# Performance work log

Hardware: AMD Instinct MI355X
Metric: run time of the kernel (lower is better)

## Reference

```python
import jax, jax.numpy as jnp
import numpy as np

B, S, D_IN, D_H, DEPTH = 4, 2048, 1024, 1024, 1024


def setup_inputs() -> dict:
    key = jax.random.key(0)
    ks = jax.random.split(key, 11)
    s = 1.0 / np.sqrt(D_IN)
    sh = 1.0 / np.sqrt(D_H)
    return {
        "query": jax.random.normal(ks[0], (B, S, D_IN), jnp.float32),
        "keys": jax.random.normal(ks[1], (B, S, D_IN), jnp.float32),
        "values": jax.random.normal(ks[2], (B, S, D_IN), jnp.float32),
        "Wq": jax.random.normal(ks[3], (D_IN, D_H), jnp.float32) * s,
        "bq": jax.random.normal(ks[4], (D_H,), jnp.float32) * s,
        "Wk": jax.random.normal(ks[5], (D_IN, D_H), jnp.float32) * s,
        "bk": jax.random.normal(ks[6], (D_H,), jnp.float32) * s,
        "Wv": jax.random.normal(ks[7], (D_IN, D_H), jnp.float32) * s,
        "bv": jax.random.normal(ks[8], (D_H,), jnp.float32) * s,
        "Wd": jax.random.normal(ks[9], (D_H, DEPTH), jnp.float32) * sh,
        "bd": jax.random.normal(ks[10], (DEPTH,), jnp.float32) * sh,
    }


def reference(query, keys, values, Wq, bq, Wk, bk, Wv, bv, Wd, bd):
    q = jnp.einsum("bsd,dh->bsh", query, Wq) + bq
    k = jnp.einsum("bsd,dh->bsh", keys, Wk) + bk
    v = jnp.einsum("bsd,dh->bsh", values, Wv) + bv
    # NOTE: source has no 1/sqrt(d) scaling
    scores = jnp.einsum("bqh,bkh->bqk", q, k)  # [B, S, S]
    attn = jax.nn.softmax(scores, axis=-1)
    attended = jnp.einsum("bqk,bkh->bqh", attn, v)
    return jnp.einsum("bsh,hd->bsd", attended, Wd) + bd
```

## Files before the change

kernel.cpp:

```cpp
#include <hip/hip_runtime.h>
#include <stdint.h>

#define BM 128
#define BN 128
#define BK 64
#define TILE_ELEMS (128 * 64)

typedef _Float16 f16;
typedef __attribute__((ext_vector_type(8))) _Float16 f16x8;
typedef __attribute__((ext_vector_type(4))) _Float16 f16x4;
typedef __attribute__((ext_vector_type(4))) float floatx4;

static __device__ __forceinline__ void async_load16(const void* g, void* l) {
    __builtin_amdgcn_global_load_lds(
        (const __attribute__((address_space(1))) unsigned int*)g,
        (__attribute__((address_space(3))) unsigned int*)l, 16, 0, 0);
}

static __device__ __forceinline__ void stage_tile(const f16* src, int ld, f16* lds, int tid) {
    int lane = tid & 63;
    int wbase = (tid >> 6) * 64;
#pragma unroll
    for (int t = 0; t < 4; ++t) {
        int c = wbase + t * 256 + lane;
        int r = c >> 3, ck = c & 7;
        const f16* gp = src + (size_t)r * ld + ((ck ^ (r & 7)) << 3);
        f16* lp = lds + (size_t)(wbase + t * 256) * 8;
        async_load16(gp, lp);
    }
}

static __device__ __forceinline__ f16x8 frag(const f16* lds, int row, int kblk) {
    return *(const f16x8*)(lds + (((row << 3) + (kblk ^ (row & 7))) << 3));
}

template <int CMODE>
static __device__ __forceinline__ void gemm_body(
    f16* As, f16* Bs,
    const f16* Ap, int lda, long long a_zoff,
    const f16* Bp, int ldb, long long b_zoff,
    void* Cp, int ldc, long long c_zoff,
    const float* bias, int K, int z)
{
    int tid = threadIdx.x;
    int lane = tid & 63;
    int wid = tid >> 6;
    int wm = wid >> 1, wn = wid & 1;

    int gx = gridDim.x;
    int nwg = gx * gridDim.y;
    int bid = blockIdx.y * gx + blockIdx.x;
    if ((nwg & 7) == 0) {
        int chunk = nwg >> 3;
        bid = (bid & 7) * chunk + (bid >> 3);
    }
    int bx = bid % gx;
    int by = bid / gx;

    size_t row0 = (size_t)by * BM;
    size_t col0 = (size_t)bx * BN;

    floatx4 acc[4][4];
#pragma unroll
    for (int i = 0; i < 4; ++i)
#pragma unroll
        for (int j = 0; j < 4; ++j) acc[i][j] = floatx4{0.f, 0.f, 0.f, 0.f};

    const f16* a0 = Ap + (size_t)z * a_zoff + row0 * lda;
    const f16* b0 = Bp + (size_t)z * b_zoff + col0 * ldb;

    int quad = lane >> 4, mr = lane & 15;

    for (int k0 = 0; k0 < K; k0 += BK) {
        __syncthreads();
        stage_tile(a0 + k0, lda, As, tid);
        stage_tile(b0 + k0, ldb, Bs, tid);
        __syncthreads();

#pragma unroll
        for (int s = 0; s < 2; ++s) {
            f16x8 ah[4];
#pragma unroll
            for (int i = 0; i < 4; ++i) ah[i] = frag(As, wm * 64 + i * 16 + mr, s * 4 + quad);
#pragma unroll
            for (int j = 0; j < 4; ++j) {
                f16x8 bh = frag(Bs, wn * 64 + j * 16 + mr, s * 4 + quad);
#pragma unroll
                for (int i = 0; i < 4; ++i)
                    acc[i][j] = __builtin_amdgcn_mfma_f32_16x16x32_f16(ah[i], bh, acc[i][j], 0, 0, 0);
            }
        }
    }

#pragma unroll
    for (int i = 0; i < 4; ++i) {
#pragma unroll
        for (int j = 0; j < 4; ++j) {
#pragma unroll
            for (int r = 0; r < 4; ++r) {
                size_t rr = row0 + (size_t)(wm * 64 + i * 16 + quad * 4 + r);
                size_t cc = col0 + (size_t)(wn * 64 + j * 16 + mr);
                float v = acc[i][j][r];
                if (bias) v += bias[cc];
                if constexpr (CMODE == 0) {
                    float* C = (float*)Cp + (size_t)z * c_zoff;
                    C[rr * ldc + cc] = v;
                } else if constexpr (CMODE == 1) {
                    f16* C = (f16*)Cp + (size_t)z * c_zoff;
                    C[rr * ldc + cc] = (f16)v;
                } else {
                    f16* C = (f16*)Cp;
                    size_t b = rr >> 11, s = rr & 2047;
                    C[((b << 10) + cc) * 2048 + s] = (f16)v;
                }
            }
        }
    }
}

#define DECL_SMEM                                        \
    __shared__ __align__(16) f16 smem[2 * TILE_ELEMS];   \
    f16* As = smem;                                      \
    f16* Bs = smem + TILE_ELEMS;

__global__ __launch_bounds__(256, 2) void g_qkv(const f16* x, const f16* W,
                                                f16* qk, f16* vT,
                                                const float* bq, const float* bk,
                                                const float* bv, int D, long long ten) {
    DECL_SMEM
    int z = blockIdx.z;
    const float* bias = (z == 0) ? bq : (z == 1) ? bk : bv;
    if (z < 2) {
        gemm_body<1>(As, Bs, x + (size_t)z * ten, D, 0, W + (size_t)z * D * D, D, 0,
                     qk + (size_t)z * ten, D, 0, bias, D, 0);
    } else {
        gemm_body<3>(As, Bs, x + (size_t)2 * ten, D, 0, W + (size_t)2 * D * D, D, 0,
                     vT, 0, 0, bias, D, 0);
    }
}
__global__ __launch_bounds__(256, 2) void g_scores(const f16* A, int lda, long long az,
                                                   const f16* B, int ldb, long long bz,
                                                   float* C, int ldc, long long cz, int K) {
    DECL_SMEM
    gemm_body<0>(As, Bs, A, lda, az, B, ldb, bz, C, ldc, cz, nullptr, K, blockIdx.z);
}
__global__ __launch_bounds__(256, 2) void g_attnv(const f16* A, int lda, long long az,
                                                  const f16* B, int ldb, long long bz,
                                                  f16* C, int ldc, long long cz, int K) {
    DECL_SMEM
    gemm_body<1>(As, Bs, A, lda, az, B, ldb, bz, C, ldc, cz, nullptr, K, blockIdx.z);
}
__global__ __launch_bounds__(256, 2) void g_out(const f16* A, int lda, const f16* B, int ldb,
                                                float* C, int ldc, const float* bias, int K) {
    DECL_SMEM
    gemm_body<0>(As, Bs, A, lda, 0, B, ldb, 0, C, ldc, 0, bias, K, 0);
}

__global__ __launch_bounds__(256) void cvt_f16(const float* q, const float* k, const float* v,
                                               f16* dst, long long ten) {
    int z = blockIdx.y;
    const float* src = (z == 0) ? q : (z == 1) ? k : v;
    size_t i = ((size_t)blockIdx.x * 256 + threadIdx.x) * 4;
    float4 x = *(const float4*)(src + i);
    f16x4 h = {(f16)x.x, (f16)x.y, (f16)x.z, (f16)x.w};
    *(f16x4*)(dst + (size_t)z * ten + i) = h;
}

__global__ __launch_bounds__(256) void wtrans(const float* Wq, const float* Wk,
                                              const float* Wv, const float* Wd,
                                              f16* T, int n) {
    __shared__ float tile[32][33];
    int z = blockIdx.z;
    const float* W = (z == 0) ? Wq : (z == 1) ? Wk : (z == 2) ? Wv : Wd;
    f16* Tz = T + (size_t)z * n * n;
    int bx = blockIdx.x * 32;
    int by = blockIdx.y * 32;
    int tx = threadIdx.x & 31;
    int ty = threadIdx.x >> 5;
    for (int r = ty; r < 32; r += 8) tile[r][tx] = W[(size_t)(by + r) * n + bx + tx];
    __syncthreads();
    for (int r = ty; r < 32; r += 8) Tz[(size_t)(bx + r) * n + by + tx] = (f16)tile[tx][r];
}

__global__ __launch_bounds__(256) void softmax_k(float* scores) {
    size_t row = blockIdx.x;
    float* rp = scores + row * 2048;
    int tid = threadIdx.x;
    int lane = tid & 63, w = tid >> 6;
    float x[8];
    float mx = -3.4e38f;
#pragma unroll
    for (int i = 0; i < 8; ++i) {
        x[i] = rp[tid + i * 256];
        mx = fmaxf(mx, x[i]);
    }
#pragma unroll
    for (int o = 32; o > 0; o >>= 1) mx = fmaxf(mx, __shfl_xor(mx, o, 64));
    __shared__ float redm[4];
    __shared__ float reds[4];
    if (lane == 0) redm[w] = mx;
    __syncthreads();
    mx = fmaxf(fmaxf(redm[0], redm[1]), fmaxf(redm[2], redm[3]));
    float s = 0.f;
#pragma unroll
    for (int i = 0; i < 8; ++i) {
        x[i] = __expf(x[i] - mx);
        s += x[i];
    }
#pragma unroll
    for (int o = 32; o > 0; o >>= 1) s += __shfl_xor(s, o, 64);
    if (lane == 0) reds[w] = s;
    __syncthreads();
    s = reds[0] + reds[1] + reds[2] + reds[3];
    float inv = 1.f / s;
    f16* op = (f16*)rp;
#pragma unroll
    for (int i = 0; i < 8; ++i) op[tid + i * 256] = (f16)(x[i] * inv);
}

extern "C" void kernel_launch(void* const* d_in, const int* in_sizes, int n_in,
                              void* d_out, int out_size, void* d_ws, size_t ws_size,
                              hipStream_t stream) {
    const float* query  = (const float*)d_in[0];
    const float* keys   = (const float*)d_in[1];
    const float* values = (const float*)d_in[2];
    const float* Wq = (const float*)d_in[3];
    const float* bq = (const float*)d_in[4];
    const float* Wk = (const float*)d_in[5];
    const float* bk = (const float*)d_in[6];
    const float* Wv = (const float*)d_in[7];
    const float* bv = (const float*)d_in[8];
    const float* Wd = (const float*)d_in[9];
    const float* bd = (const float*)d_in[10];
    float* out = (float*)d_out;

    const int S = 2048, D = 1024, NB = 4;
    const size_t TEN = (size_t)NB * S * D;

    char* p = (char*)d_ws;
    auto alloc = [&](size_t bytes) {
        char* r = p;
        p += (bytes + 255) & ~(size_t)255;
        return r;
    };
    f16* x3  = (f16*)alloc(TEN * 2 * 3);
    f16* q16 = (f16*)alloc(TEN * 2 * 2);
    f16* k16 = q16 + TEN;
    f16* vT  = (f16*)alloc(TEN * 2);
    f16* WT  = (f16*)alloc((size_t)D * D * 2 * 4);
    float* scores = (float*)p;
    long long avail = (long long)ws_size - (long long)(p - (char*)d_ws);
    long long sbytes = (long long)S * S * 4;
    int g = (avail >= 4 * sbytes) ? 4 : (avail >= 2 * sbytes) ? 2 : 1;
    f16* att = x3;

    dim3 blk(256);
    cvt_f16<<<dim3((unsigned)(TEN / 1024), 3), blk, 0, stream>>>(query, keys, values, x3, TEN);
    wtrans<<<dim3(D / 32, D / 32, 4), blk, 0, stream>>>(Wq, Wk, Wv, Wd, WT, D);

    g_qkv<<<dim3(D / BN, (NB * S) / BM, 3), blk, 0, stream>>>(
        x3, WT, q16, vT, bq, bk, bv, D, (long long)TEN);

    for (int g0 = 0; g0 < NB; g0 += g) {
        int gz = (NB - g0 < g) ? (NB - g0) : g;
        dim3 sgrid(S / BN, S / BM, gz);
        g_scores<<<sgrid, blk, 0, stream>>>(
            q16 + (size_t)g0 * S * D, D, (long long)S * D,
            k16 + (size_t)g0 * S * D, D, (long long)S * D,
            scores, S, (long long)S * S, D);
        softmax_k<<<dim3((unsigned)(gz * S)), blk, 0, stream>>>(scores);
        dim3 agrid(D / BN, S / BM, gz);
        g_attnv<<<agrid, blk, 0, stream>>>(
            (const f16*)scores, 2 * S, (long long)S * 2 * S,
            vT + (size_t)g0 * D * S, S, (long long)D * S,
            att + (size_t)g0 * S * D, D, (long long)S * D, S);
    }

    g_out<<<dim3(D / BN, (NB * S) / BM, 1), blk, 0, stream>>>(att, D, WT + (size_t)3 * D * D, D,
                                                              out, D, bd, D);
}
```

Baseline: 359.4 us.

## Use 256x256 GEMM tiles with 8 waves and double-buffered LDS prefetch

Every GEMM kernel now uses 256x256 output tiles computed by 512 threads (8 waves, 2x4 layout), each wave holding a 128x64 accumulator block. The K loop double-buffers A and B tiles in LDS. It spreads the async global-to-LDS loads for the next tile across four compute phases and raises wave priority around the MFMA bursts. The goal is to hide global load latency and raise arithmetic intensity per LDS byte. In exchange it uses 128KB of LDS per block, and there are fewer workgroups: the output projection has only 128 blocks, which may leave CUs idle.

Measured after the change: 446.0 us. +24.1%, slower.

```diff
diff --git a/kernel.cpp b/kernel.cpp
--- a/kernel.cpp
+++ b/kernel.cpp
@@ -1,36 +1,34 @@
 #include <hip/hip_runtime.h>
 #include <stdint.h>
 
-#define BM 128
-#define BN 128
+#define BM 256
+#define BN 256
 #define BK 64
-#define TILE_ELEMS (128 * 64)
+#define TSTRIDE 32768
 
 typedef _Float16 f16;
 typedef __attribute__((ext_vector_type(8))) _Float16 f16x8;
 typedef __attribute__((ext_vector_type(4))) _Float16 f16x4;
 typedef __attribute__((ext_vector_type(4))) float floatx4;
 
+#define SBAR() asm volatile("s_barrier" ::: "memory")
+#define WAITV0() asm volatile("s_waitcnt vmcnt(0)" ::: "memory")
+
 static __device__ __forceinline__ void async_load16(const void* g, void* l) {
     __builtin_amdgcn_global_load_lds(
         (const __attribute__((address_space(1))) unsigned int*)g,
         (__attribute__((address_space(3))) unsigned int*)l, 16, 0, 0);
 }
 
-static __device__ __forceinline__ void stage_tile(const f16* src, int ld, f16* lds, int tid) {
-    int lane = tid & 63;
-    int wbase = (tid >> 6) * 64;
-#pragma unroll
-    for (int t = 0; t < 4; ++t) {
-        int c = wbase + t * 256 + lane;
-        int r = c >> 3, ck = c & 7;
-        const f16* gp = src + (size_t)r * ld + ((ck ^ (r & 7)) << 3);
-        f16* lp = lds + (size_t)(wbase + t * 256) * 8;
-        async_load16(gp, lp);
-    }
-}
-
-static __device__ __forceinline__ f16x8 frag(const f16* lds, int row, int kblk) {
+static __device__ __forceinline__ void stage256(const f16* src, int ld, f16* lds, int tid, int chunk) {
+    int c = (chunk << 9) + tid;
+    int r = c >> 3, ck = c & 7;
+    const f16* gp = src + (size_t)r * ld + ((ck ^ (r & 7)) << 3);
+    f16* lp = lds + (size_t)((chunk << 9) + (tid & ~63)) * 8;
+    async_load16(gp, lp);
+}
+
+static __device__ __forceinline__ f16x8 frag256(const f16* lds, int row, int kblk) {
     return *(const f16x8*)(lds + (((row << 3) + (kblk ^ (row & 7))) << 3));
 }
 
@@ -45,7 +43,7 @@
     int tid = threadIdx.x;
     int lane = tid & 63;
     int wid = tid >> 6;
-    int wm = wid >> 1, wn = wid & 1;
+    int wm = wid >> 2, wn = wid & 3;
 
     int gx = gridDim.x;
     int nwg = gx * gridDim.y;
@@ -56,13 +54,12 @@
     }
     int bx = bid % gx;
     int by = bid / gx;
-
     size_t row0 = (size_t)by * BM;
     size_t col0 = (size_t)bx * BN;
 
-    floatx4 acc[4][4];
-#pragma unroll
-    for (int i = 0; i < 4; ++i)
+    floatx4 acc[8][4];
+#pragma unroll
+    for (int i = 0; i < 8; ++i)
 #pragma unroll
         for (int j = 0; j < 4; ++j) acc[i][j] = floatx4{0.f, 0.f, 0.f, 0.f};
 
@@ -70,35 +67,75 @@
     const f16* b0 = Bp + (size_t)z * b_zoff + col0 * ldb;
 
     int quad = lane >> 4, mr = lane & 15;
-
-    for (int k0 = 0; k0 < K; k0 += BK) {
-        __syncthreads();
-        stage_tile(a0 + k0, lda, As, tid);
-        stage_tile(b0 + k0, ldb, Bs, tid);
-        __syncthreads();
-
-#pragma unroll
-        for (int s = 0; s < 2; ++s) {
-            f16x8 ah[4];
-#pragma unroll
-            for (int i = 0; i < 4; ++i) ah[i] = frag(As, wm * 64 + i * 16 + mr, s * 4 + quad);
-#pragma unroll
-            for (int j = 0; j < 4; ++j) {
-                f16x8 bh = frag(Bs, wn * 64 + j * 16 + mr, s * 4 + quad);
+    int NT = K >> 6;
+
+#pragma unroll
+    for (int c = 0; c < 4; ++c) stage256(a0, lda, As, tid, c);
+#pragma unroll
+    for (int c = 0; c < 4; ++c) stage256(b0, ldb, Bs, tid, c);
+    WAITV0();
+    SBAR();
+
+    for (int kt = 0; kt < NT; ++kt) {
+        int cur = kt & 1;
+        f16* Acur = As + cur * TSTRIDE;
+        f16* Bcur = Bs + cur * TSTRIDE;
+        f16* Anxt = As + (cur ^ 1) * TSTRIDE;
+        f16* Bnxt = Bs + (cur ^ 1) * TSTRIDE;
+        const f16* an = a0 + (size_t)(kt + 1) * BK;
+        const f16* bn = b0 + (size_t)(kt + 1) * BK;
+        bool pf = (kt + 1 < NT);
+
+#pragma unroll
+        for (int p = 0; p < 4; ++p) {
+            const int mh = p >> 1, nh = p & 1;
+            f16x8 af[2][4], bf[2][2];
+#pragma unroll
+            for (int s = 0; s < 2; ++s) {
 #pragma unroll
                 for (int i = 0; i < 4; ++i)
-                    acc[i][j] = __builtin_amdgcn_mfma_f32_16x16x32_f16(ah[i], bh, acc[i][j], 0, 0, 0);
+                    af[s][i] = frag256(Acur, wm * 128 + mh * 64 + i * 16 + mr, s * 4 + quad);
+#pragma unroll
+                for (int j = 0; j < 2; ++j)
+                    bf[s][j] = frag256(Bcur, wn * 64 + nh * 32 + j * 16 + mr, s * 4 + quad);
             }
+            if (pf) {
+                if (p == 0) {
+                    stage256(an, lda, Anxt, tid, 0);
+                    stage256(an, lda, Anxt, tid, 1);
+                    stage256(an, lda, Anxt, tid, 2);
+                } else if (p == 1) {
+                    stage256(an, lda, Anxt, tid, 3);
+                    stage256(bn, ldb, Bnxt, tid, 0);
+                    stage256(bn, ldb, Bnxt, tid, 1);
+                } else if (p == 2) {
+                    stage256(bn, ldb, Bnxt, tid, 2);
+                    stage256(bn, ldb, Bnxt, tid, 3);
+                }
+            }
+            SBAR();
+            __builtin_amdgcn_s_setprio(1);
+#pragma unroll
+            for (int s = 0; s < 2; ++s)
+#pragma unroll
+                for (int j = 0; j < 2; ++j)
+#pragma unroll
+                    for (int i = 0; i < 4; ++i)
+                        acc[mh * 4 + i][nh * 2 + j] = __builtin_amdgcn_mfma_f32_16x16x32_f16(
+                            af[s][i], bf[s][j], acc[mh * 4 + i][nh * 2 + j], 0, 0, 0);
+            __builtin_amdgcn_s_setprio(0);
+            if (p == 3 && pf) WAITV0();
+            SBAR();
         }
     }
 
 #pragma unroll
-    for (int i = 0; i < 4; ++i) {
+    for (int i = 0; i < 8; ++i) {
 #pragma unroll
         for (int j = 0; j < 4; ++j) {
 #pragma unroll
             for (int r = 0; r < 4; ++r) {
-                size_t rr = row0 + (size_t)(wm * 64 + i * 16 + quad * 4 + r);
+                size_t rr = row0 + (size_t)(wm * 128 + i * 16 + quad * 4 + r);
                 size_t cc = col0 + (size_t)(wn * 64 + j * 16 + mr);
                 float v = acc[i][j][r];
                 if (bias) v += bias[cc];
@@ -118,12 +155,12 @@
     }
 }
 
-#define DECL_SMEM                                        \
-    __shared__ __align__(16) f16 smem[2 * TILE_ELEMS];   \
-    f16* As = smem;                                      \
-    f16* Bs = smem + TILE_ELEMS;
-
-__global__ __launch_bounds__(256, 2) void g_qkv(const f16* x, const f16* W,
+#define DECL_SMEM                                      \
+    __shared__ __align__(16) f16 smem[2 * TSTRIDE];    \
+    f16* As = smem;                                    \
+    f16* Bs = smem + 16384;
+
+__global__ __launch_bounds__(512, 2) void g_qkv(const f16* x, const f16* W,
                                                 f16* qk, f16* vT,
                                                 const float* bq, const float* bk,
                                                 const float* bv, int D, long long ten) {
@@ -138,19 +175,19 @@
                      vT, 0, 0, bias, D, 0);
     }
 }
-__global__ __launch_bounds__(256, 2) void g_scores(const f16* A, int lda, long long az,
+__global__ __launch_bounds__(512, 2) void g_scores(const f16* A, int lda, long long az,
                                                    const f16* B, int ldb, long long bz,
                                                    float* C, int ldc, long long cz, int K) {
     DECL_SMEM
     gemm_body<0>(As, Bs, A, lda, az, B, ldb, bz, C, ldc, cz, nullptr, K, blockIdx.z);
 }
-__global__ __launch_bounds__(256, 2) void g_attnv(const f16* A, int lda, long long az,
+__global__ __launch_bounds__(512, 2) void g_attnv(const f16* A, int lda, long long az,
                                                   const f16* B, int ldb, long long bz,
                                                   f16* C, int ldc, long long cz, int K) {
     DECL_SMEM
     gemm_body<1>(As, Bs, A, lda, az, B, ldb, bz, C, ldc, cz, nullptr, K, blockIdx.z);
 }
-__global__ __launch_bounds__(256, 2) void g_out(const f16* A, int lda, const f16* B, int ldb,
+__global__ __launch_bounds__(512, 2) void g_out(const f16* A, int lda, const f16* B, int ldb,
                                                 float* C, int ldc, const float* bias, int K) {
     DECL_SMEM
     gemm_body<0>(As, Bs, A, lda, 0, B, ldb, 0, C, ldc, 0, bias, K, 0);
@@ -255,27 +292,28 @@
     f16* att = x3;
 
     dim3 blk(256);
+    dim3 blk512(512);
     cvt_f16<<<dim3((unsigned)(TEN / 1024), 3), blk, 0, stream>>>(query, keys, values, x3, TEN);
     wtrans<<<dim3(D / 32, D / 32, 4), blk, 0, stream>>>(Wq, Wk, Wv, Wd, WT, D);
 
-    g_qkv<<<dim3(D / BN, (NB * S) / BM, 3), blk, 0, stream>>>(
+    g_qkv<<<dim3(D / BN, (NB * S) / BM, 3), blk512, 0, stream>>>(
         x3, WT, q16, vT, bq, bk, bv, D, (long long)TEN);
 
     for (int g0 = 0; g0 < NB; g0 += g) {
         int gz = (NB - g0 < g) ? (NB - g0) : g;
         dim3 sgrid(S / BN, S / BM, gz);
-        g_scores<<<sgrid, blk, 0, stream>>>(
+        g_scores<<<sgrid, blk512, 0, stream>>>(
             q16 + (size_t)g0 * S * D, D, (long long)S * D,
             k16 + (size_t)g0 * S * D, D, (long long)S * D,
             scores, S, (long long)S * S, D);
         softmax_k<<<dim3((unsigned)(gz * S)), blk, 0, stream>>>(scores);
         dim3 agrid(D / BN, S / BM, gz);
-        g_attnv<<<agrid, blk, 0, stream>>>(
+        g_attnv<<<agrid, blk512, 0, stream>>>(
             (const f16*)scores, 2 * S, (long long)S * 2 * S,
             vT + (size_t)g0 * D * S, S, (long long)D * S,
             att + (size_t)g0 * S * D, D, (long long)S * D, S);
     }
 
-    g_out<<<dim3(D / BN, (NB * S) / BM, 1), blk, 0, stream>>>(att, D, WT + (size_t)3 * D * D, D,
-                                                              out, D, bd, D);
-}
+    g_out<<<dim3(D / BN, (NB * S) / BM, 1), blk512, 0, stream>>>(att, D, WT + (size_t)3 * D * D, D,
+                                                                 out, D, bd, D);
+}
```

## Triple-buffer GEMM K-loop with async LDS loads and 256x128 tiles

Applied to the files above, without the earlier changes.

Replaces the two-barrier, single-buffer K loop with a three-stage ring of LDS buffers. Global-to-LDS loads for tile k+2 are issued while tile k is being computed, and explicit vmcnt waits plus a single s_barrier per iteration gate each stage. The block tile grows to 256x128 with 512 threads (8 waves), and fragments are preloaded before an MFMA burst that runs at raised wave priority. This aims to hide global load latency and halve barrier count, at the cost of about 147KB of LDS per block, which limits occupancy to one block per CU and halves the grid size.

Result: slower. 383.7 us (+6.8%).

```diff
diff --git a/kernel.cpp b/kernel.cpp
--- a/kernel.cpp
+++ b/kernel.cpp
@@ -1,33 +1,34 @@
 #include <hip/hip_runtime.h>
 #include <stdint.h>
 
-#define BM 128
+#define BM 256
 #define BN 128
 #define BK 64
-#define TILE_ELEMS (128 * 64)
+#define ATILE (BM * BK)
+#define BTILE (BN * BK)
+#define BUFSTRIDE (ATILE + BTILE)
 
 typedef _Float16 f16;
 typedef __attribute__((ext_vector_type(8))) _Float16 f16x8;
 typedef __attribute__((ext_vector_type(4))) _Float16 f16x4;
 typedef __attribute__((ext_vector_type(4))) float floatx4;
 
+#define SBAR() asm volatile("s_barrier" ::: "memory")
+#define WAITV6() asm volatile("s_waitcnt vmcnt(6)" ::: "memory")
+#define WAITV0() asm volatile("s_waitcnt vmcnt(0)" ::: "memory")
+
 static __device__ __forceinline__ void async_load16(const void* g, void* l) {
     __builtin_amdgcn_global_load_lds(
         (const __attribute__((address_space(1))) unsigned int*)g,
         (__attribute__((address_space(3))) unsigned int*)l, 16, 0, 0);
 }
 
-static __device__ __forceinline__ void stage_tile(const f16* src, int ld, f16* lds, int tid) {
-    int lane = tid & 63;
-    int wbase = (tid >> 6) * 64;
-#pragma unroll
-    for (int t = 0; t < 4; ++t) {
-        int c = wbase + t * 256 + lane;
-        int r = c >> 3, ck = c & 7;
-        const f16* gp = src + (size_t)r * ld + ((ck ^ (r & 7)) << 3);
-        f16* lp = lds + (size_t)(wbase + t * 256) * 8;
-        async_load16(gp, lp);
-    }
+static __device__ __forceinline__ void stage_unit(const f16* src, int ld, f16* lds, int tid, int u) {
+    int c = (u << 9) + tid;
+    int r = c >> 3, ck = c & 7;
+    const f16* gp = src + (size_t)r * ld + ((ck ^ (r & 7)) << 3);
+    f16* lp = lds + (size_t)((u << 9) + (tid & ~63)) * 8;
+    async_load16(gp, lp);
 }
 
 static __device__ __forceinline__ f16x8 frag(const f16* lds, int row, int kblk) {
@@ -36,7 +37,7 @@
 
 template <int CMODE>
 static __device__ __forceinline__ void gemm_body(
-    f16* As, f16* Bs,
+    f16* smem,
     const f16* Ap, int lda, long long a_zoff,
     const f16* Bp, int ldb, long long b_zoff,
     void* Cp, int ldc, long long c_zoff,
@@ -56,7 +57,6 @@
     }
     int bx = bid % gx;
     int by = bid / gx;
-
     size_t row0 = (size_t)by * BM;
     size_t col0 = (size_t)bx * BN;
 
@@ -70,25 +70,54 @@
     const f16* b0 = Bp + (size_t)z * b_zoff + col0 * ldb;
 
     int quad = lane >> 4, mr = lane & 15;
-
-    for (int k0 = 0; k0 < K; k0 += BK) {
-        __syncthreads();
-        stage_tile(a0 + k0, lda, As, tid);
-        stage_tile(b0 + k0, ldb, Bs, tid);
-        __syncthreads();
-
+    int NT = K >> 6;
+
+    auto issue_tile = [&](int kt) {
+        f16* Ab = smem + (kt % 3) * BUFSTRIDE;
+        f16* Bb = Ab + ATILE;
+        const f16* an = a0 + (size_t)kt * BK;
+        const f16* bn = b0 + (size_t)kt * BK;
+        stage_unit(an, lda, Ab, tid, 0);
+        stage_unit(an, lda, Ab, tid, 1);
+        stage_unit(an, lda, Ab, tid, 2);
+        stage_unit(an, lda, Ab, tid, 3);
+        stage_unit(bn, ldb, Bb, tid, 0);
+        stage_unit(bn, ldb, Bb, tid, 1);
+    };
+
+    issue_tile(0);
+    issue_tile(1);
+    WAITV6();
+    SBAR();
+
+    for (int kt = 0; kt < NT; ++kt) {
+        f16* Ac = smem + (kt % 3) * BUFSTRIDE;
+        f16* Bc = Ac + ATILE;
+        if (kt + 2 < NT) issue_tile(kt + 2);
+
+        f16x8 af[2][4], bf[2][4];
 #pragma unroll
         for (int s = 0; s < 2; ++s) {
-            f16x8 ah[4];
-#pragma unroll
-            for (int i = 0; i < 4; ++i) ah[i] = frag(As, wm * 64 + i * 16 + mr, s * 4 + quad);
-#pragma unroll
-            for (int j = 0; j < 4; ++j) {
-                f16x8 bh = frag(Bs, wn * 64 + j * 16 + mr, s * 4 + quad);
+#pragma unroll
+            for (int i = 0; i < 4; ++i)
+                af[s][i] = frag(Ac, wm * 64 + i * 16 + mr, s * 4 + quad);
+#pragma unroll
+            for (int j = 0; j < 4; ++j)
+                bf[s][j] = frag(Bc, wn * 64 + j * 16 + mr, s * 4 + quad);
+        }
+        __builtin_amdgcn_s_setprio(1);
+#pragma unroll
+        for (int s = 0; s < 2; ++s)
+#pragma unroll
+            for (int j = 0; j < 4; ++j)
 #pragma unroll
                 for (int i = 0; i < 4; ++i)
-                    acc[i][j] = __builtin_amdgcn_mfma_f32_16x16x32_f16(ah[i], bh, acc[i][j], 0, 0, 0);
-            }
+                    acc[i][j] = __builtin_amdgcn_mfma_f32_16x16x32_f16(af[s][i], bf[s][j], acc[i][j], 0, 0, 0);
+        __builtin_amdgcn_s_setprio(0);
+
+        if (kt + 1 < NT) {
+            if (kt + 2 < NT) WAITV6(); else WAITV0();
+            SBAR();
         }
     }
 
@@ -118,12 +147,9 @@
     }
 }
 
-#define DECL_SMEM                                        \
-    __shared__ __align__(16) f16 smem[2 * TILE_ELEMS];   \
-    f16* As = smem;                                      \
-    f16* Bs = smem + TILE_ELEMS;
-
-__global__ __launch_bounds__(256, 2) void g_qkv(const f16* x, const f16* W,
+#define DECL_SMEM __shared__ __align__(16) f16 smem[3 * BUFSTRIDE];
+
+__global__ __launch_bounds__(512, 2) void g_qkv(const f16* x, const f16* W,
                                                 f16* qk, f16* vT,
                                                 const float* bq, const float* bk,
                                                 const float* bv, int D, long long ten) {
@@ -131,29 +157,29 @@
     int z = blockIdx.z;
     const float* bias = (z == 0) ? bq : (z == 1) ? bk : bv;
     if (z < 2) {
-        gemm_body<1>(As, Bs, x + (size_t)z * ten, D, 0, W + (size_t)z * D * D, D, 0,
+        gemm_body<1>(smem, x + (size_t)z * ten, D, 0, W + (size_t)z * D * D, D, 0,
                      qk + (size_t)z * ten, D, 0, bias, D, 0);
     } else {
-        gemm_body<3>(As, Bs, x + (size_t)2 * ten, D, 0, W + (size_t)2 * D * D, D, 0,
+        gemm_body<3>(smem, x + (size_t)2 * ten, D, 0, W + (size_t)2 * D * D, D, 0,
                      vT, 0, 0, bias, D, 0);
     }
 }
-__global__ __launch_bounds__(256, 2) void g_scores(const f16* A, int lda, long long az,
+__global__ __launch_bounds__(512, 2) void g_scores(const f16* A, int lda, long long az,
                                                    const f16* B, int ldb, long long bz,
                                                    float* C, int ldc, long long cz, int K) {
     DECL_SMEM
-    gemm_body<0>(As, Bs, A, lda, az, B, ldb, bz, C, ldc, cz, nullptr, K, blockIdx.z);
-}
-__global__ __launch_bounds__(256, 2) void g_attnv(const f16* A, int lda, long long az,
+    gemm_body<0>(smem, A, lda, az, B, ldb, bz, C, ldc, cz, nullptr, K, blockIdx.z);
+}
+__global__ __launch_bounds__(512, 2) void g_attnv(const f16* A, int lda, long long az,
                                                   const f16* B, int ldb, long long bz,
                                                   f16* C, int ldc, long long cz, int K) {
     DECL_SMEM
-    gemm_body<1>(As, Bs, A, lda, az, B, ldb, bz, C, ldc, cz, nullptr, K, blockIdx.z);
-}
-__global__ __launch_bounds__(256, 2) void g_out(const f16* A, int lda, const f16* B, int ldb,
+    gemm_body<1>(smem, A, lda, az, B, ldb, bz, C, ldc, cz, nullptr, K, blockIdx.z);
+}
+__global__ __launch_bounds__(512, 2) void g_out(const f16* A, int lda, const f16* B, int ldb,
                                                 float* C, int ldc, const float* bias, int K) {
     DECL_SMEM
-    gemm_body<0>(As, Bs, A, lda, 0, B, ldb, 0, C, ldc, 0, bias, K, 0);
+    gemm_body<0>(smem, A, lda, 0, B, ldb, 0, C, ldc, 0, bias, K, 0);
 }
 
 __global__ __launch_bounds__(256) void cvt_f16(const float* q, const float* k, const float* v,
@@ -255,27 +281,28 @@
     f16* att = x3;
 
     dim3 blk(256);
+    dim3 blk512(512);
     cvt_f16<<<dim3((unsigned)(TEN / 1024), 3), blk, 0, stream>>>(query, keys, values, x3, TEN);
     wtrans<<<dim3(D / 32, D / 32, 4), blk, 0, stream>>>(Wq, Wk, Wv, Wd, WT, D);
 
-    g_qkv<<<dim3(D / BN, (NB * S) / BM, 3), blk, 0, stream>>>(
+    g_qkv<<<dim3(D / BN, (NB * S) / BM, 3), blk512, 0, stream>>>(
         x3, WT, q16, vT, bq, bk, bv, D, (long long)TEN);
 
     for (int g0 = 0; g0 < NB; g0 += g) {
         int gz = (NB - g0 < g) ? (NB - g0) : g;
         dim3 sgrid(S / BN, S / BM, gz);
-        g_scores<<<sgrid, blk, 0, stream>>>(
+        g_scores<<<sgrid, blk512, 0, stream>>>(
             q16 + (size_t)g0 * S * D, D, (long long)S * D,
             k16 + (size_t)g0 * S * D, D, (long long)S * D,
             scores, S, (long long)S * S, D);
         softmax_k<<<dim3((unsigned)(gz * S)), blk, 0, stream>>>(scores);
         dim3 agrid(D / BN, S / BM, gz);
-        g_attnv<<<agrid, blk, 0, stream>>>(
+        g_attnv<<<agrid, blk512, 0, stream>>>(
             (const f16*)scores, 2 * S, (long long)S * 2 * S,
             vT + (size_t)g0 * D * S, S, (long long)D * S,
             att + (size_t)g0 * S * D, D, (long long)S * D, S);
     }
 
-    g_out<<<dim3(D / BN, (NB * S) / BM, 1), blk, 0, stream>>>(att, D, WT + (size_t)3 * D * D, D,
-                                                              out, D, bd, D);
-}
+    g_out<<<dim3(D / BN, (NB * S) / BM, 1), blk512, 0, stream>>>(att, D, WT + (size_t)3 * D * D, D,
+                                                                 out, D, bd, D);
+}
```

## Double-buffer GEMM LDS tiles and vectorize softmax row loads/stores

Applied to the files above, without the earlier changes.

The shared GEMM body now uses two LDS buffers, issuing async global-to-LDS loads for the next K tile while MFMAs run on the current one, with one barrier per iteration instead of two. LDS use per block doubles to 64 KB, which may limit the two-blocks-per-CU occupancy target. The softmax kernel also switches to contiguous per-thread float4 loads and f16x4 stores instead of strided scalar accesses. The in-place f16 write over the fp32 row is safe because of the barriers between the read and the write.

Result: slower. 374.3 us (+4.2%).

```diff
diff --git a/kernel.cpp b/kernel.cpp
--- a/kernel.cpp
+++ b/kernel.cpp
@@ -36,7 +36,7 @@
 
 template <int CMODE>
 static __device__ __forceinline__ void gemm_body(
-    f16* As, f16* Bs,
+    f16* smem,
     const f16* Ap, int lda, long long a_zoff,
     const f16* Bp, int ldb, long long b_zoff,
     void* Cp, int ldc, long long c_zoff,
@@ -71,25 +71,34 @@
 
     int quad = lane >> 4, mr = lane & 15;
 
-    for (int k0 = 0; k0 < K; k0 += BK) {
-        __syncthreads();
-        stage_tile(a0 + k0, lda, As, tid);
-        stage_tile(b0 + k0, ldb, Bs, tid);
-        __syncthreads();
+    stage_tile(a0, lda, smem, tid);
+    stage_tile(b0, ldb, smem + TILE_ELEMS, tid);
+    __syncthreads();
+
+    int kt = 0;
+    for (int k0 = 0; k0 < K; k0 += BK, ++kt) {
+        f16* Ac = smem + (kt & 1) * (2 * TILE_ELEMS);
+        f16* Bc = Ac + TILE_ELEMS;
+        if (k0 + BK < K) {
+            f16* An = smem + ((kt & 1) ^ 1) * (2 * TILE_ELEMS);
+            stage_tile(a0 + k0 + BK, lda, An, tid);
+            stage_tile(b0 + k0 + BK, ldb, An + TILE_ELEMS, tid);
+        }
 
 #pragma unroll
         for (int s = 0; s < 2; ++s) {
             f16x8 ah[4];
 #pragma unroll
-            for (int i = 0; i < 4; ++i) ah[i] = frag(As, wm * 64 + i * 16 + mr, s * 4 + quad);
+            for (int i = 0; i < 4; ++i) ah[i] = frag(Ac, wm * 64 + i * 16 + mr, s * 4 + quad);
 #pragma unroll
             for (int j = 0; j < 4; ++j) {
-                f16x8 bh = frag(Bs, wn * 64 + j * 16 + mr, s * 4 + quad);
+                f16x8 bh = frag(Bc, wn * 64 + j * 16 + mr, s * 4 + quad);
 #pragma unroll
                 for (int i = 0; i < 4; ++i)
                     acc[i][j] = __builtin_amdgcn_mfma_f32_16x16x32_f16(ah[i], bh, acc[i][j], 0, 0, 0);
             }
         }
+        __syncthreads();
     }
 
 #pragma unroll
@@ -118,10 +127,7 @@
     }
 }
 
-#define DECL_SMEM                                        \
-    __shared__ __align__(16) f16 smem[2 * TILE_ELEMS];   \
-    f16* As = smem;                                      \
-    f16* Bs = smem + TILE_ELEMS;
+#define DECL_SMEM __shared__ __align__(16) f16 smem[4 * TILE_ELEMS];
 
 __global__ __launch_bounds__(256, 2) void g_qkv(const f16* x, const f16* W,
                                                 f16* qk, f16* vT,
@@ -131,10 +137,10 @@
     int z = blockIdx.z;
     const float* bias = (z == 0) ? bq : (z == 1) ? bk : bv;
     if (z < 2) {
-        gemm_body<1>(As, Bs, x + (size_t)z * ten, D, 0, W + (size_t)z * D * D, D, 0,
+        gemm_body<1>(smem, x + (size_t)z * ten, D, 0, W + (size_t)z * D * D, D, 0,
                      qk + (size_t)z * ten, D, 0, bias, D, 0);
     } else {
-        gemm_body<3>(As, Bs, x + (size_t)2 * ten, D, 0, W + (size_t)2 * D * D, D, 0,
+        gemm_body<3>(smem, x + (size_t)2 * ten, D, 0, W + (size_t)2 * D * D, D, 0,
                      vT, 0, 0, bias, D, 0);
     }
 }
@@ -142,18 +148,18 @@
                                                    const f16* B, int ldb, long long bz,
                                                    float* C, int ldc, long long cz, int K) {
     DECL_SMEM
-    gemm_body<0>(As, Bs, A, lda, az, B, ldb, bz, C, ldc, cz, nullptr, K, blockIdx.z);
+    gemm_body<0>(smem, A, lda, az, B, ldb, bz, C, ldc, cz, nullptr, K, blockIdx.z);
 }
 __global__ __launch_bounds__(256, 2) void g_attnv(const f16* A, int lda, long long az,
                                                   const f16* B, int ldb, long long bz,
                                                   f16* C, int ldc, long long cz, int K) {
     DECL_SMEM
-    gemm_body<1>(As, Bs, A, lda, az, B, ldb, bz, C, ldc, cz, nullptr, K, blockIdx.z);
+    gemm_body<1>(smem, A, lda, az, B, ldb, bz, C, ldc, cz, nullptr, K, blockIdx.z);
 }
 __global__ __launch_bounds__(256, 2) void g_out(const f16* A, int lda, const f16* B, int ldb,
                                                 float* C, int ldc, const float* bias, int K) {
     DECL_SMEM
-    gemm_body<0>(As, Bs, A, lda, 0, B, ldb, 0, C, ldc, 0, bias, K, 0);
+    gemm_body<0>(smem, A, lda, 0, B, ldb, 0, C, ldc, 0, bias, K, 0);
 }
 
 __global__ __launch_bounds__(256) void cvt_f16(const float* q, const float* k, const float* v,
@@ -187,13 +193,12 @@
     float* rp = scores + row * 2048;
     int tid = threadIdx.x;
     int lane = tid & 63, w = tid >> 6;
-    float x[8];
+    const float4* rp4 = (const float4*)(rp + (size_t)tid * 8);
+    float4 a = rp4[0], b = rp4[1];
+    float x[8] = {a.x, a.y, a.z, a.w, b.x, b.y, b.z, b.w};
     float mx = -3.4e38f;
 #pragma unroll
-    for (int i = 0; i < 8; ++i) {
-        x[i] = rp[tid + i * 256];
-        mx = fmaxf(mx, x[i]);
-    }
+    for (int i = 0; i < 8; ++i) mx = fmaxf(mx, x[i]);
 #pragma unroll
     for (int o = 32; o > 0; o >>= 1) mx = fmaxf(mx, __shfl_xor(mx, o, 64));
     __shared__ float redm[4];
@@ -213,9 +218,11 @@
     __syncthreads();
     s = reds[0] + reds[1] + reds[2] + reds[3];
     float inv = 1.f / s;
-    f16* op = (f16*)rp;
-#pragma unroll
-    for (int i = 0; i < 8; ++i) op[tid + i * 256] = (f16)(x[i] * inv);
+    f16* op = (f16*)rp + (size_t)tid * 8;
+    f16x4 h0 = {(f16)(x[0] * inv), (f16)(x[1] * inv), (f16)(x[2] * inv), (f16)(x[3] * inv)};
+    f16x4 h1 = {(f16)(x[4] * inv), (f16)(x[5] * inv), (f16)(x[6] * inv), (f16)(x[7] * inv)};
+    *(f16x4*)op = h0;
+    *(f16x4*)(op + 4) = h1;
 }
 
 extern "C" void kernel_launch(void* const* d_in, const int* in_sizes, int n_in,
```
